# Kernel tuning notes

Hardware: AMD Instinct MI355X
Metric: run time of the kernel (lower is better)

The kernel has to match this reference:

```python
import jax, jax.numpy as jnp
import numpy as np

N = 50000      # nodes
E = 800000     # edges (before self-loops)
IN = 256       # input features
H = 8          # heads
C = 32         # hidden channels per head
OUT = 40       # classes
NEG_SLOPE = 0.2


def setup_inputs() -> dict:
    key = jax.random.key(0)
    ks = jax.random.split(key, 12)
    sd = lambda k, sh: (jax.random.normal(k, sh, jnp.float32) * 0.05)
    return {
        "x": jax.random.normal(ks[0], (N, IN), jnp.float32),
        "edge_index": jax.random.randint(ks[1], (2, E), 0, N),
        "W1": sd(ks[2], (IN, H * C)),
        "a_src1": sd(ks[3], (H, C)),
        "a_dst1": sd(ks[4], (H, C)),
        "b1": jnp.zeros((C,), jnp.float32),
        "W2": sd(ks[5], (C, H * C)),
        "a_src2": sd(ks[6], (H, C)),
        "a_dst2": sd(ks[7], (H, C)),
        "b2": jnp.zeros((C,), jnp.float32),
        "Wo": sd(ks[8], (C, OUT)),
        "bo": jnp.zeros((OUT,), jnp.float32),
    }


def gat_layer(x, src, dst, n, W, a_src, a_dst, b):
    # x: [N, F]; src/dst: [E'] (self-loops included). concat=False -> mean over heads.
    h = (x @ W).reshape(n, H, C)                       # [N, H, C]
    alpha_src = jnp.sum(h * a_src, axis=-1)            # [N, H]
    alpha_dst = jnp.sum(h * a_dst, axis=-1)            # [N, H]
    e = alpha_src[src] + alpha_dst[dst]                # [E', H]
    e = jnp.where(e > 0, e, NEG_SLOPE * e)             # leaky_relu
    # segment softmax over incoming edges of each dst node
    m = jax.ops.segment_max(e, dst, num_segments=n)    # [N, H]
    ex = jnp.exp(e - m[dst])                           # [E', H]
    s = jax.ops.segment_sum(ex, dst, num_segments=n)   # [N, H]
    alpha = ex / s[dst]                                # [E', H]
    msg = alpha[:, :, None] * h[src]                   # [E', H, C]
    out = jax.ops.segment_sum(msg, dst, num_segments=n)  # [N, H, C]
    return out.mean(axis=1) + b                        # [N, C]


def reference(x, edge_index, W1, a_src1, a_dst1, b1, W2, a_src2, a_dst2, b2, Wo, bo):
    n = x.shape[0]
    loops = jnp.arange(n, dtype=edge_index.dtype)
    src = jnp.concatenate([edge_index[0], loops])      # add self-loops (PyG default)
    dst = jnp.concatenate([edge_index[1], loops])
    h = gat_layer(x, src, dst, n, W1, a_src1, a_dst1, b1)
    h = jax.nn.elu(h)                                  # dropout skipped (eval)
    h = gat_layer(h, src, dst, n, W2, a_src2, a_dst2, b2)
    h = jax.nn.elu(h)
    logits = h @ Wo + bo
    return jax.nn.log_softmax(logits, axis=1)
```

## Files before the change

### kernel.cpp

```cpp
#include <hip/hip_runtime.h>
#include <math.h>

#define N_NODES 50000
#define N_PAD   50016
#define N_EDGES 800000
#define E_TOT   (N_EDGES + N_NODES)
#define F_IN    256
#define NHEAD   8
#define CH      32
#define HC      256
#define OUT_C   40
#define NEG_SLOPE 0.2f
#define SCAN_BLOCKS ((N_NODES + 255) / 256)
#define G_XCVT  ((N_NODES * F_IN / 8 + 255) / 256)
#define G_WCVT  ((HC * F_IN + 255) / 256)
#define G_WCVT2 ((HC * CH + 255) / 256)

typedef unsigned short u16;
typedef unsigned int   u32;
typedef unsigned char  u8;
typedef __attribute__((ext_vector_type(8))) short bf16x8;
typedef __attribute__((ext_vector_type(4))) float f32x4;
typedef __attribute__((ext_vector_type(2))) float f32x2;

__device__ __forceinline__ u16 f2bf(float f) {
    union { u32 u; float f; } x; x.f = f;
    u32 u = x.u;
    return (u16)((u + 0x7fffu + ((u >> 16) & 1u)) >> 16);
}
__device__ __forceinline__ float bflo(u32 v) {
    union { u32 u; float f; } x; x.u = v << 16; return x.f;
}
__device__ __forceinline__ u8 f2fp8(float f) {
    return (u8)(__builtin_amdgcn_cvt_pk_fp8_f32(f, f, 0, false) & 0xff);
}


__global__ __launch_bounds__(256) void cvt_kernel(const float* __restrict__ x,
        u16* __restrict__ xb, const float* __restrict__ W1, u16* __restrict__ Wt,
        const float* __restrict__ W2, u16* __restrict__ W2t) {
    int b = blockIdx.x;
    if (b < G_XCVT) {
        int t = b * 256 + threadIdx.x;
        if (t >= N_NODES * F_IN / 8) return;
        const float4* xp = (const float4*)x + (size_t)t * 2;
        float4 v0 = xp[0], v1 = xp[1];
        uint4 o;
        o.x = (u32)f2bf(v0.x) | ((u32)f2bf(v0.y) << 16);
        o.y = (u32)f2bf(v0.z) | ((u32)f2bf(v0.w) << 16);
        o.z = (u32)f2bf(v1.x) | ((u32)f2bf(v1.y) << 16);
        o.w = (u32)f2bf(v1.z) | ((u32)f2bf(v1.w) << 16);
        ((uint4*)xb)[t] = o;
    } else if (b < G_XCVT + G_WCVT) {
        int t = (b - G_XCVT) * 256 + threadIdx.x;
        int n = t & 255, k = t >> 8;
        Wt[(size_t)n * F_IN + k] = f2bf(W1[(size_t)k * HC + n]);
    } else {
        int t = (b - G_XCVT - G_WCVT) * 256 + threadIdx.x;
        if (t >= HC * CH) return;
        int n = t & 255, k = t >> 8;
        W2t[(size_t)n * CH + k] = f2bf(W2[(size_t)k * HC + n]);
    }
}

__global__ __launch_bounds__(256) void gemm1_mfma(const u16* __restrict__ xb,
        const u16* __restrict__ Wt, u8* __restrict__ ht8) {
    const int row0 = blockIdx.x * 32;
    const int t    = threadIdx.x;
    const int wave = t >> 6;
    const int lane = t & 63;
    const int l16  = lane & 15;
    const int quad = lane >> 4;
    const int nb   = wave * 64;

    f32x4 acc[2][4];
    #pragma unroll
    for (int m = 0; m < 2; ++m)
        #pragma unroll
        for (int n = 0; n < 4; ++n) acc[m][n] = (f32x4){0.f, 0.f, 0.f, 0.f};

    const u16* a0p = xb + (size_t)(row0 + l16) * F_IN;
    const u16* a1p = a0p + 16 * F_IN;
    const u16* bp  = Wt + (size_t)(nb + l16) * F_IN;

    #pragma unroll 1
    for (int k0 = 0; k0 < F_IN; k0 += 32) {
        const int ko = k0 + quad * 8;
        bf16x8 a0 = *(const bf16x8*)(a0p + ko);
        bf16x8 a1 = *(const bf16x8*)(a1p + ko);
        bf16x8 b0 = *(const bf16x8*)(bp + 0 * 16 * F_IN + ko);
        bf16x8 b1 = *(const bf16x8*)(bp + 1 * 16 * F_IN + ko);
        bf16x8 b2 = *(const bf16x8*)(bp + 2 * 16 * F_IN + ko);
        bf16x8 b3 = *(const bf16x8*)(bp + 3 * 16 * F_IN + ko);
        acc[0][0] = __builtin_amdgcn_mfma_f32_16x16x32_bf16(a0, b0, acc[0][0], 0, 0, 0);
        acc[0][1] = __builtin_amdgcn_mfma_f32_16x16x32_bf16(a0, b1, acc[0][1], 0, 0, 0);
        acc[0][2] = __builtin_amdgcn_mfma_f32_16x16x32_bf16(a0, b2, acc[0][2], 0, 0, 0);
        acc[0][3] = __builtin_amdgcn_mfma_f32_16x16x32_bf16(a0, b3, acc[0][3], 0, 0, 0);
        acc[1][0] = __builtin_amdgcn_mfma_f32_16x16x32_bf16(a1, b0, acc[1][0], 0, 0, 0);
        acc[1][1] = __builtin_amdgcn_mfma_f32_16x16x32_bf16(a1, b1, acc[1][1], 0, 0, 0);
        acc[1][2] = __builtin_amdgcn_mfma_f32_16x16x32_bf16(a1, b2, acc[1][2], 0, 0, 0);
        acc[1][3] = __builtin_amdgcn_mfma_f32_16x16x32_bf16(a1, b3, acc[1][3], 0, 0, 0);
    }

    #pragma unroll
    for (int m = 0; m < 2; ++m) {
        #pragma unroll
        for (int r = 0; r < 4; ++r) {
            int row = row0 + m * 16 + quad * 4 + r;
            if (row < N_NODES) {
                u8* hr = ht8 + (size_t)row * HC;
                #pragma unroll
                for (int n = 0; n < 4; ++n) {
                    int col = nb + n * 16 + l16;
                    hr[col] = f2fp8(acc[m][n][r]);
                }
            }
        }
    }
}

__global__ __launch_bounds__(256) void gemm2_mfma(const u16* __restrict__ hmb,
        const u16* __restrict__ W2t, u8* __restrict__ ht8) {
    const int row0 = blockIdx.x * 32;
    const int t    = threadIdx.x;
    const int wave = t >> 6;
    const int lane = t & 63;
    const int l16  = lane & 15;
    const int quad = lane >> 4;
    const int nb   = wave * 64;
    const int ko   = quad * 8;

    const u16* a0p = hmb + (size_t)(row0 + l16) * CH;
    const u16* a1p = a0p + 16 * CH;
    const u16* bp  = W2t + (size_t)(nb + l16) * CH;

    bf16x8 a0 = *(const bf16x8*)(a0p + ko);
    bf16x8 a1 = *(const bf16x8*)(a1p + ko);
    bf16x8 b0 = *(const bf16x8*)(bp + 0 * 16 * CH + ko);
    bf16x8 b1 = *(const bf16x8*)(bp + 1 * 16 * CH + ko);
    bf16x8 b2 = *(const bf16x8*)(bp + 2 * 16 * CH + ko);
    bf16x8 b3 = *(const bf16x8*)(bp + 3 * 16 * CH + ko);

    f32x4 z = (f32x4){0.f, 0.f, 0.f, 0.f};
    f32x4 acc[2][4];
    acc[0][0] = __builtin_amdgcn_mfma_f32_16x16x32_bf16(a0, b0, z, 0, 0, 0);
    acc[0][1] = __builtin_amdgcn_mfma_f32_16x16x32_bf16(a0, b1, z, 0, 0, 0);
    acc[0][2] = __builtin_amdgcn_mfma_f32_16x16x32_bf16(a0, b2, z, 0, 0, 0);
    acc[0][3] = __builtin_amdgcn_mfma_f32_16x16x32_bf16(a0, b3, z, 0, 0, 0);
    acc[1][0] = __builtin_amdgcn_mfma_f32_16x16x32_bf16(a1, b0, z, 0, 0, 0);
    acc[1][1] = __builtin_amdgcn_mfma_f32_16x16x32_bf16(a1, b1, z, 0, 0, 0);
    acc[1][2] = __builtin_amdgcn_mfma_f32_16x16x32_bf16(a1, b2, z, 0, 0, 0);
    acc[1][3] = __builtin_amdgcn_mfma_f32_16x16x32_bf16(a1, b3, z, 0, 0, 0);

    #pragma unroll
    for (int m = 0; m < 2; ++m) {
        #pragma unroll
        for (int r = 0; r < 4; ++r) {
            int row = row0 + m * 16 + quad * 4 + r;
            if (row < N_NODES) {
                u8* hr = ht8 + (size_t)row * HC;
                #pragma unroll
                for (int n = 0; n < 4; ++n) {
                    int col = nb + n * 16 + l16;
                    hr[col] = f2fp8(acc[m][n][r]);
                }
            }
        }
    }
}

__global__ __launch_bounds__(256) void alpha_t_kernel(const u8* __restrict__ ht8,
        const float* __restrict__ a_src, const float* __restrict__ a_dst,
        float* __restrict__ asrc, float* __restrict__ adst) {
    __shared__ float sas[HC], sad[HC];
    for (int i = threadIdx.x; i < HC; i += 256) {
        sas[i] = a_src[i];
        sad[i] = a_dst[i];
    }
    __syncthreads();
    int node = blockIdx.x * 256 + threadIdx.x;
    if (node >= N_NODES) return;
    const uint2* hp = (const uint2*)(ht8 + (size_t)node * HC);
    float s1[NHEAD], s2[NHEAD];
    #pragma unroll
    for (int h = 0; h < NHEAD; ++h) {
        float t1 = 0.f, t2 = 0.f;
        #pragma unroll
        for (int i = 0; i < 4; ++i) {
            uint2 v = hp[h * 4 + i];
            f32x2 p01 = __builtin_amdgcn_cvt_pk_f32_fp8(v.x, false);
            f32x2 p23 = __builtin_amdgcn_cvt_pk_f32_fp8(v.x, true);
            f32x2 p45 = __builtin_amdgcn_cvt_pk_f32_fp8(v.y, false);
            f32x2 p67 = __builtin_amdgcn_cvt_pk_f32_fp8(v.y, true);
            const float* s1p = &sas[h * CH + i * 8];
            const float* s2p = &sad[h * CH + i * 8];
            t1 += p01.x * s1p[0] + p01.y * s1p[1] + p23.x * s1p[2] + p23.y * s1p[3]
                + p45.x * s1p[4] + p45.y * s1p[5] + p67.x * s1p[6] + p67.y * s1p[7];
            t2 += p01.x * s2p[0] + p01.y * s2p[1] + p23.x * s2p[2] + p23.y * s2p[3]
                + p45.x * s2p[4] + p45.y * s2p[5] + p67.x * s2p[6] + p67.y * s2p[7];
        }
        s1[h] = t1; s2[h] = t2;
    }
    float4* o1 = (float4*)(asrc + (size_t)node * NHEAD);
    float4* o2 = (float4*)(adst + (size_t)node * NHEAD);
    o1[0] = make_float4(s1[0], s1[1], s1[2], s1[3]);
    o1[1] = make_float4(s1[4], s1[5], s1[6], s1[7]);
    o2[0] = make_float4(s2[0], s2[1], s2[2], s2[3]);
    o2[1] = make_float4(s2[4], s2[5], s2[6], s2[7]);
}

__global__ __launch_bounds__(256) void deg_kernel(const int* __restrict__ ei,
        int* __restrict__ deg) {
    int j = blockIdx.x * 256 + threadIdx.x;
    if (j >= E_TOT) return;
    int dst = (j < N_EDGES) ? ei[N_EDGES + j] : (j - N_EDGES);
    atomicAdd(&deg[dst], 1);
}

__device__ __forceinline__ int wave_incl_scan(int v, int lane) {
    #pragma unroll
    for (int d = 1; d < 64; d <<= 1) {
        int u = __shfl_up(v, d, 64);
        if (lane >= d) v += u;
    }
    return v;
}

__global__ __launch_bounds__(256) void scan1_kernel(const int* __restrict__ deg,
        int* __restrict__ rowptr, int* __restrict__ partials) {
    const int t    = blockIdx.x * 256 + threadIdx.x;
    const int lane = threadIdx.x & 63;
    const int wid  = threadIdx.x >> 6;
    int v = (t < N_NODES) ? deg[t] : 0;
    int inc = wave_incl_scan(v, lane);
    __shared__ int wtot[4];
    if (lane == 63) wtot[wid] = inc;
    __syncthreads();
    int woff = 0;
    #pragma unroll
    for (int i = 0; i < 4; ++i) woff += (i < wid) ? wtot[i] : 0;
    if (t < N_NODES) rowptr[t] = inc - v + woff;
    if (threadIdx.x == 255) partials[blockIdx.x] = woff + inc;
}

__global__ __launch_bounds__(256) void scan2_kernel(int* __restrict__ partials) {
    const int t    = threadIdx.x;
    const int lane = t & 63;
    const int wid  = t >> 6;
    int v = (t < SCAN_BLOCKS) ? partials[t] : 0;
    int inc = wave_incl_scan(v, lane);
    __shared__ int wtot[4];
    if (lane == 63) wtot[wid] = inc;
    __syncthreads();
    int woff = 0;
    #pragma unroll
    for (int i = 0; i < 4; ++i) woff += (i < wid) ? wtot[i] : 0;
    __syncthreads();
    if (t < SCAN_BLOCKS) partials[t] = inc - v + woff;
}

__global__ __launch_bounds__(256) void scan3_kernel(int* __restrict__ rowptr,
        int* __restrict__ cursor, const int* __restrict__ partials) {
    const int t = blockIdx.x * 256 + threadIdx.x;
    if (t < N_NODES) {
        int v = rowptr[t] + partials[blockIdx.x];
        rowptr[t] = v;
        cursor[t] = v;
    } else if (t == N_NODES) {
        rowptr[N_NODES] = E_TOT;
    }
}

__global__ __launch_bounds__(256) void scatter_kernel(const int* __restrict__ ei,
        int* __restrict__ cursor, int* __restrict__ csr_src) {
    int j = blockIdx.x * 256 + threadIdx.x;
    if (j >= E_TOT) return;
    int src, dst;
    if (j < N_EDGES) { src = ei[j]; dst = ei[N_EDGES + j]; }
    else             { src = j - N_EDGES; dst = src; }
    int pos = atomicAdd(&cursor[dst], 1);
    csr_src[pos] = src;
}

__global__ __launch_bounds__(256) void attn_kernel(const int* __restrict__ rowptr,
        const int* __restrict__ csr_src, const float* __restrict__ asrc,
        const float* __restrict__ adst, const u8* __restrict__ ht8,
        const float* __restrict__ b, u16* __restrict__ out) {
    const int wid = (blockIdx.x * 256 + threadIdx.x) >> 6;
    if (wid >= N_NODES) return;
    const int dst  = wid;
    const int lane = threadIdx.x & 63;
    const int q    = lane >> 4;
    const int l16  = lane & 15;
    const int h    = l16 >> 1;
    const float ad_own = adst[dst * NHEAD + h];

    float acc[16];
    #pragma unroll
    for (int i = 0; i < 16; ++i) acc[i] = 0.f;
    float wsum = 0.f;

    auto consume = [&](float as_, const uint4& hv) {
        float x = as_ + ad_own;
        x = x > 0.f ? x : NEG_SLOPE * x;
        float w = __expf(x);
        wsum += w;
        f32x2 d;
        d = __builtin_amdgcn_cvt_pk_f32_fp8(hv.x, false); acc[ 0] += w * d.x; acc[ 1] += w * d.y;
        d = __builtin_amdgcn_cvt_pk_f32_fp8(hv.x, true ); acc[ 2] += w * d.x; acc[ 3] += w * d.y;
        d = __builtin_amdgcn_cvt_pk_f32_fp8(hv.y, false); acc[ 4] += w * d.x; acc[ 5] += w * d.y;
        d = __builtin_amdgcn_cvt_pk_f32_fp8(hv.y, true ); acc[ 6] += w * d.x; acc[ 7] += w * d.y;
        d = __builtin_amdgcn_cvt_pk_f32_fp8(hv.z, false); acc[ 8] += w * d.x; acc[ 9] += w * d.y;
        d = __builtin_amdgcn_cvt_pk_f32_fp8(hv.z, true ); acc[10] += w * d.x; acc[11] += w * d.y;
        d = __builtin_amdgcn_cvt_pk_f32_fp8(hv.w, false); acc[12] += w * d.x; acc[13] += w * d.y;
        d = __builtin_amdgcn_cvt_pk_f32_fp8(hv.w, true ); acc[14] += w * d.x; acc[15] += w * d.y;
    };

    const int p0 = rowptr[dst], p1 = rowptr[dst + 1];
    const int boff = l16 * 16;

    float asA = 0.f, asB = 0.f;
    uint4 hvA = make_uint4(0u, 0u, 0u, 0u), hvB = make_uint4(0u, 0u, 0u, 0u);
    int eA = p0 + q;
    int eB = eA + 4;
    if (eA < p1) {
        int s = csr_src[eA];
        asA = asrc[s * NHEAD + h];
        hvA = *(const uint4*)(ht8 + (size_t)s * HC + boff);
    }
    if (eB < p1) {
        int s = csr_src[eB];
        asB = asrc[s * NHEAD + h];
        hvB = *(const uint4*)(ht8 + (size_t)s * HC + boff);
    }

    while (eA < p1) {
        consume(asA, hvA);
        if (eA + 8 < p1) {
            int s = csr_src[eA + 8];
            asA = asrc[s * NHEAD + h];
            hvA = *(const uint4*)(ht8 + (size_t)s * HC + boff);
        }
        if (eB < p1) consume(asB, hvB);
        if (eB + 8 < p1) {
            int s = csr_src[eB + 8];
            asB = asrc[s * NHEAD + h];
            hvB = *(const uint4*)(ht8 + (size_t)s * HC + boff);
        }
        eA += 8; eB += 8;
    }

    #pragma unroll
    for (int i = 0; i < 16; ++i) {
        acc[i] += __shfl_xor(acc[i], 16, 64);
        acc[i] += __shfl_xor(acc[i], 32, 64);
    }
    wsum += __shfl_xor(wsum, 16, 64);
    wsum += __shfl_xor(wsum, 32, 64);

    float winv = 1.0f / wsum;
    #pragma unroll
    for (int i = 0; i < 16; ++i) acc[i] *= winv;

    #pragma unroll
    for (int i = 0; i < 16; ++i) {
        acc[i] += __shfl_xor(acc[i], 2, 64);
        acc[i] += __shfl_xor(acc[i], 4, 64);
        acc[i] += __shfl_xor(acc[i], 8, 64);
    }

    if (lane < 2) {
        const int c0 = lane * 16;
        const float4* bp4 = (const float4*)(b + c0);
        float4 b0 = bp4[0], b1 = bp4[1], b2 = bp4[2], b3 = bp4[3];
        float bb[16] = {b0.x, b0.y, b0.z, b0.w, b1.x, b1.y, b1.z, b1.w,
                        b2.x, b2.y, b2.z, b2.w, b3.x, b3.y, b3.z, b3.w};
        u32 d[8];
        #pragma unroll
        for (int i = 0; i < 8; ++i) {
            float v0 = acc[2 * i]     * 0.125f + bb[2 * i];
            float v1 = acc[2 * i + 1] * 0.125f + bb[2 * i + 1];
            v0 = v0 > 0.f ? v0 : (__expf(v0) - 1.f);
            v1 = v1 > 0.f ? v1 : (__expf(v1) - 1.f);
            d[i] = (u32)f2bf(v0) | ((u32)f2bf(v1) << 16);
        }
        uint4* op = (uint4*)(out + (size_t)dst * CH + c0);
        op[0] = make_uint4(d[0], d[1], d[2], d[3]);
        op[1] = make_uint4(d[4], d[5], d[6], d[7]);
    }
}

__global__ __launch_bounds__(256) void out_kernel(const u16* __restrict__ hf,
        const float* __restrict__ Wo, const float* __restrict__ bo,
        float* __restrict__ out) {
    const int wave = threadIdx.x >> 6;
    const int lane = threadIdx.x & 63;
    const int n    = blockIdx.x * 4 + wave;
    __shared__ float hs[4][CH];
    if (n < N_NODES && lane < CH) hs[wave][lane] = bflo((u32)hf[n * CH + lane]);
    __syncthreads();
    if (n >= N_NODES) return;
    float logit = -INFINITY;
    if (lane < OUT_C) {
        float a = bo[lane];
        #pragma unroll
        for (int k = 0; k < CH; ++k) a += hs[wave][k] * Wo[k * OUT_C + lane];
        logit = a;
    }
    float m = logit;
    #pragma unroll
    for (int off = 32; off; off >>= 1) m = fmaxf(m, __shfl_xor(m, off, 64));
    float ex = (lane < OUT_C) ? __expf(logit - m) : 0.f;
    float ssum = ex;
    #pragma unroll
    for (int off = 32; off; off >>= 1) ssum += __shfl_xor(ssum, off, 64);
    if (lane < OUT_C) out[(size_t)n * OUT_C + lane] = logit - m - __logf(ssum);
}

extern "C" void kernel_launch(void* const* d_in, const int* in_sizes, int n_in,
                              void* d_out, int out_size, void* d_ws, size_t ws_size,
                              hipStream_t stream) {
    const float* x      = (const float*)d_in[0];
    const int*   ei     = (const int*)  d_in[1];
    const float* W1     = (const float*)d_in[2];
    const float* a_src1 = (const float*)d_in[3];
    const float* a_dst1 = (const float*)d_in[4];
    const float* b1     = (const float*)d_in[5];
    const float* W2     = (const float*)d_in[6];
    const float* a_src2 = (const float*)d_in[7];
    const float* a_dst2 = (const float*)d_in[8];
    const float* b2     = (const float*)d_in[9];
    const float* Wo     = (const float*)d_in[10];
    const float* bo     = (const float*)d_in[11];
    float* out = (float*)d_out;

    char* ws = (char*)d_ws;
    size_t off = 0;
    auto carve = [&](size_t bytes) { char* p = ws + off; off += (bytes + 255) & ~(size_t)255; return p; };
    u8*    ht8     = (u8*)   carve((size_t)N_NODES * HC);
    u16*   xb      = (u16*)  carve((size_t)N_PAD * F_IN * 2);
    u16*   Wt      = (u16*)  carve((size_t)HC * F_IN * 2);
    u16*   W2t     = (u16*)  carve((size_t)HC * CH * 2);
    float* asrc    = (float*)carve((size_t)N_NODES * NHEAD * 4);
    float* adst    = (float*)carve((size_t)N_NODES * NHEAD * 4);
    u16*   hmid    = (u16*)  carve((size_t)N_PAD * CH * 2);
    u16*   hout    = (u16*)  carve((size_t)N_NODES * CH * 2);
    int*   deg     = (int*)  carve((size_t)N_NODES * 4);
    int*   rowptr  = (int*)  carve((size_t)(N_NODES + 1) * 4);
    int*   cursor  = (int*)  carve((size_t)N_NODES * 4);
    int*   csr_src = (int*)  carve((size_t)E_TOT * 4);
    int*   partials= (int*)  carve((size_t)SCAN_BLOCKS * 4);

    const int g_cvt   = G_XCVT + G_WCVT + G_WCVT2;
    const int g_gemm  = (N_NODES + 31) / 32;
    const int g_node  = (N_NODES + 255) / 256;
    const int g_edge  = (E_TOT + 255) / 256;
    const int g_attn  = (N_NODES * 64 + 255) / 256;
    const int g_out   = (N_NODES + 3) / 4;

    cvt_kernel<<<g_cvt, 256, 0, stream>>>(x, xb, W1, Wt, W2, W2t);
    (void)hipMemsetAsync(deg, 0, (size_t)N_NODES * 4, stream);
    deg_kernel<<<g_edge, 256, 0, stream>>>(ei, deg);
    scan1_kernel<<<SCAN_BLOCKS, 256, 0, stream>>>(deg, rowptr, partials);
    scan2_kernel<<<1, 256, 0, stream>>>(partials);
    scan3_kernel<<<SCAN_BLOCKS, 256, 0, stream>>>(rowptr, cursor, partials);
    scatter_kernel<<<g_edge, 256, 0, stream>>>(ei, cursor, csr_src);

    gemm1_mfma<<<g_gemm, 256, 0, stream>>>(xb, Wt, ht8);
    alpha_t_kernel<<<g_node, 256, 0, stream>>>(ht8, a_src1, a_dst1, asrc, adst);
    attn_kernel<<<g_attn, 256, 0, stream>>>(rowptr, csr_src, asrc, adst, ht8, b1, hmid);

    gemm2_mfma<<<g_gemm, 256, 0, stream>>>(hmid, W2t, ht8);
    alpha_t_kernel<<<g_node, 256, 0, stream>>>(ht8, a_src2, a_dst2, asrc, adst);
    attn_kernel<<<g_attn, 256, 0, stream>>>(rowptr, csr_src, asrc, adst, ht8, b2, hout);

    out_kernel<<<g_out, 256, 0, stream>>>(hout, Wo, bo, out);
}
```

Measured before the change: 394.4 us.

## Fuse degree count into convert kernel, use 16-bit CSR indices, pack attention FMAs

The edge-degree atomic count now runs as extra blocks inside the input conversion kernel, which removes one launch and lets the two independent jobs overlap. CSR source indices are stored as 16-bit values, halving the index traffic that the attention gathers read; this depends on the node count fitting below 65536. The attention loop becomes a fixed-trip loop with two prefetched edges per step. Missing edges are padded with a very large negative score so their weight comes out as zero, and the feature accumulation uses packed two-wide FMAs to cut VALU instructions.

Measured after the change: 383.0 us. 2.9% less time.

```diff
diff --git a/kernel.cpp b/kernel.cpp
--- a/kernel.cpp
+++ b/kernel.cpp
@@ -12,6 +12,7 @@
 #define OUT_C   40
 #define NEG_SLOPE 0.2f
 #define SCAN_BLOCKS ((N_NODES + 255) / 256)
+#define G_DEG   ((E_TOT + 255) / 256)
 #define G_XCVT  ((N_NODES * F_IN / 8 + 255) / 256)
 #define G_WCVT  ((HC * F_IN + 255) / 256)
 #define G_WCVT2 ((HC * CH + 255) / 256)
@@ -38,10 +39,16 @@
 
 __global__ __launch_bounds__(256) void cvt_kernel(const float* __restrict__ x,
         u16* __restrict__ xb, const float* __restrict__ W1, u16* __restrict__ Wt,
-        const float* __restrict__ W2, u16* __restrict__ W2t) {
+        const float* __restrict__ W2, u16* __restrict__ W2t,
+        const int* __restrict__ ei, int* __restrict__ deg) {
     int b = blockIdx.x;
-    if (b < G_XCVT) {
-        int t = b * 256 + threadIdx.x;
+    if (b < G_DEG) {
+        int j = b * 256 + threadIdx.x;
+        if (j >= E_TOT) return;
+        int dstn = (j < N_EDGES) ? ei[N_EDGES + j] : (j - N_EDGES);
+        atomicAdd(&deg[dstn], 1);
+    } else if (b < G_DEG + G_XCVT) {
+        int t = (b - G_DEG) * 256 + threadIdx.x;
         if (t >= N_NODES * F_IN / 8) return;
         const float4* xp = (const float4*)x + (size_t)t * 2;
         float4 v0 = xp[0], v1 = xp[1];
@@ -51,12 +58,12 @@
         o.z = (u32)f2bf(v1.x) | ((u32)f2bf(v1.y) << 16);
         o.w = (u32)f2bf(v1.z) | ((u32)f2bf(v1.w) << 16);
         ((uint4*)xb)[t] = o;
-    } else if (b < G_XCVT + G_WCVT) {
-        int t = (b - G_XCVT) * 256 + threadIdx.x;
+    } else if (b < G_DEG + G_XCVT + G_WCVT) {
+        int t = (b - G_DEG - G_XCVT) * 256 + threadIdx.x;
         int n = t & 255, k = t >> 8;
         Wt[(size_t)n * F_IN + k] = f2bf(W1[(size_t)k * HC + n]);
     } else {
-        int t = (b - G_XCVT - G_WCVT) * 256 + threadIdx.x;
+        int t = (b - G_DEG - G_XCVT - G_WCVT) * 256 + threadIdx.x;
         if (t >= HC * CH) return;
         int n = t & 255, k = t >> 8;
         W2t[(size_t)n * CH + k] = f2bf(W2[(size_t)k * HC + n]);
@@ -209,14 +216,6 @@
     o2[1] = make_float4(s2[4], s2[5], s2[6], s2[7]);
 }
 
-__global__ __launch_bounds__(256) void deg_kernel(const int* __restrict__ ei,
-        int* __restrict__ deg) {
-    int j = blockIdx.x * 256 + threadIdx.x;
-    if (j >= E_TOT) return;
-    int dst = (j < N_EDGES) ? ei[N_EDGES + j] : (j - N_EDGES);
-    atomicAdd(&deg[dst], 1);
-}
-
 __device__ __forceinline__ int wave_incl_scan(int v, int lane) {
     #pragma unroll
     for (int d = 1; d < 64; d <<= 1) {
@@ -272,18 +271,18 @@
 }
 
 __global__ __launch_bounds__(256) void scatter_kernel(const int* __restrict__ ei,
-        int* __restrict__ cursor, int* __restrict__ csr_src) {
+        int* __restrict__ cursor, u16* __restrict__ csr_src) {
     int j = blockIdx.x * 256 + threadIdx.x;
     if (j >= E_TOT) return;
     int src, dst;
     if (j < N_EDGES) { src = ei[j]; dst = ei[N_EDGES + j]; }
     else             { src = j - N_EDGES; dst = src; }
     int pos = atomicAdd(&cursor[dst], 1);
-    csr_src[pos] = src;
+    csr_src[pos] = (u16)src;
 }
 
 __global__ __launch_bounds__(256) void attn_kernel(const int* __restrict__ rowptr,
-        const int* __restrict__ csr_src, const float* __restrict__ asrc,
+        const u16* __restrict__ csr_src, const float* __restrict__ asrc,
         const float* __restrict__ adst, const u8* __restrict__ ht8,
         const float* __restrict__ b, u16* __restrict__ out) {
     const int wid = (blockIdx.x * 256 + threadIdx.x) >> 6;
@@ -294,79 +293,100 @@
     const int l16  = lane & 15;
     const int h    = l16 >> 1;
     const float ad_own = adst[dst * NHEAD + h];
-
-    float acc[16];
-    #pragma unroll
-    for (int i = 0; i < 16; ++i) acc[i] = 0.f;
+    const u8* hbase = ht8 + l16 * 16;
+
+    f32x2 acc2[8];
+    #pragma unroll
+    for (int i = 0; i < 8; ++i) acc2[i] = (f32x2){0.f, 0.f};
     float wsum = 0.f;
 
-    auto consume = [&](float as_, const uint4& hv) {
-        float x = as_ + ad_own;
-        x = x > 0.f ? x : NEG_SLOPE * x;
-        float w = __expf(x);
-        wsum += w;
-        f32x2 d;
-        d = __builtin_amdgcn_cvt_pk_f32_fp8(hv.x, false); acc[ 0] += w * d.x; acc[ 1] += w * d.y;
-        d = __builtin_amdgcn_cvt_pk_f32_fp8(hv.x, true ); acc[ 2] += w * d.x; acc[ 3] += w * d.y;
-        d = __builtin_amdgcn_cvt_pk_f32_fp8(hv.y, false); acc[ 4] += w * d.x; acc[ 5] += w * d.y;
-        d = __builtin_amdgcn_cvt_pk_f32_fp8(hv.y, true ); acc[ 6] += w * d.x; acc[ 7] += w * d.y;
-        d = __builtin_amdgcn_cvt_pk_f32_fp8(hv.z, false); acc[ 8] += w * d.x; acc[ 9] += w * d.y;
-        d = __builtin_amdgcn_cvt_pk_f32_fp8(hv.z, true ); acc[10] += w * d.x; acc[11] += w * d.y;
-        d = __builtin_amdgcn_cvt_pk_f32_fp8(hv.w, false); acc[12] += w * d.x; acc[13] += w * d.y;
-        d = __builtin_amdgcn_cvt_pk_f32_fp8(hv.w, true ); acc[14] += w * d.x; acc[15] += w * d.y;
-    };
-
     const int p0 = rowptr[dst], p1 = rowptr[dst + 1];
-    const int boff = l16 * 16;
-
-    float asA = 0.f, asB = 0.f;
+    const int nt = (p1 - p0 + 7) >> 3;
+
+    float asA = -1e30f, asB = -1e30f;
     uint4 hvA = make_uint4(0u, 0u, 0u, 0u), hvB = make_uint4(0u, 0u, 0u, 0u);
-    int eA = p0 + q;
-    int eB = eA + 4;
-    if (eA < p1) {
-        int s = csr_src[eA];
+    int e = p0 + q;
+    if (e < p1) {
+        int s = (int)csr_src[e];
         asA = asrc[s * NHEAD + h];
-        hvA = *(const uint4*)(ht8 + (size_t)s * HC + boff);
-    }
-    if (eB < p1) {
-        int s = csr_src[eB];
+        hvA = *(const uint4*)(hbase + ((size_t)s << 8));
+    }
+    if (e + 4 < p1) {
+        int s = (int)csr_src[e + 4];
         asB = asrc[s * NHEAD + h];
-        hvB = *(const uint4*)(ht8 + (size_t)s * HC + boff);
-    }
-
-    while (eA < p1) {
-        consume(asA, hvA);
-        if (eA + 8 < p1) {
-            int s = csr_src[eA + 8];
+        hvB = *(const uint4*)(hbase + ((size_t)s << 8));
+    }
+
+    for (int it = 0; it < nt; ++it) {
+        float aA = asA; uint4 hA = hvA;
+        float aB = asB; uint4 hB = hvB;
+        asA = -1e30f; asB = -1e30f;
+        if (e + 8 < p1) {
+            int s = (int)csr_src[e + 8];
             asA = asrc[s * NHEAD + h];
-            hvA = *(const uint4*)(ht8 + (size_t)s * HC + boff);
-        }
-        if (eB < p1) consume(asB, hvB);
-        if (eB + 8 < p1) {
-            int s = csr_src[eB + 8];
+            hvA = *(const uint4*)(hbase + ((size_t)s << 8));
+        }
+        if (e + 12 < p1) {
+            int s = (int)csr_src[e + 12];
             asB = asrc[s * NHEAD + h];
-            hvB = *(const uint4*)(ht8 + (size_t)s * HC + boff);
-        }
-        eA += 8; eB += 8;
-    }
-
-    #pragma unroll
-    for (int i = 0; i < 16; ++i) {
-        acc[i] += __shfl_xor(acc[i], 16, 64);
-        acc[i] += __shfl_xor(acc[i], 32, 64);
+            hvB = *(const uint4*)(hbase + ((size_t)s << 8));
+        }
+        {
+            float x = aA + ad_own;
+            x = x > 0.f ? x : NEG_SLOPE * x;
+            float w = __expf(x);
+            wsum += w;
+            f32x2 w2; w2.x = w; w2.y = w;
+            acc2[0] = __builtin_elementwise_fma(w2, __builtin_amdgcn_cvt_pk_f32_fp8(hA.x, false), acc2[0]);
+            acc2[1] = __builtin_elementwise_fma(w2, __builtin_amdgcn_cvt_pk_f32_fp8(hA.x, true ), acc2[1]);
+            acc2[2] = __builtin_elementwise_fma(w2, __builtin_amdgcn_cvt_pk_f32_fp8(hA.y, false), acc2[2]);
+            acc2[3] = __builtin_elementwise_fma(w2, __builtin_amdgcn_cvt_pk_f32_fp8(hA.y, true ), acc2[3]);
+            acc2[4] = __builtin_elementwise_fma(w2, __builtin_amdgcn_cvt_pk_f32_fp8(hA.z, false), acc2[4]);
+            acc2[5] = __builtin_elementwise_fma(w2, __builtin_amdgcn_cvt_pk_f32_fp8(hA.z, true ), acc2[5]);
+            acc2[6] = __builtin_elementwise_fma(w2, __builtin_amdgcn_cvt_pk_f32_fp8(hA.w, false), acc2[6]);
+            acc2[7] = __builtin_elementwise_fma(w2, __builtin_amdgcn_cvt_pk_f32_fp8(hA.w, true ), acc2[7]);
+        }
+        {
+            float x = aB + ad_own;
+            x = x > 0.f ? x : NEG_SLOPE * x;
+            float w = __expf(x);
+            wsum += w;
+            f32x2 w2; w2.x = w; w2.y = w;
+            acc2[0] = __builtin_elementwise_fma(w2, __builtin_amdgcn_cvt_pk_f32_fp8(hB.x, false), acc2[0]);
+            acc2[1] = __builtin_elementwise_fma(w2, __builtin_amdgcn_cvt_pk_f32_fp8(hB.x, true ), acc2[1]);
+            acc2[2] = __builtin_elementwise_fma(w2, __builtin_amdgcn_cvt_pk_f32_fp8(hB.y, false), acc2[2]);
+            acc2[3] = __builtin_elementwise_fma(w2, __builtin_amdgcn_cvt_pk_f32_fp8(hB.y, true ), acc2[3]);
+            acc2[4] = __builtin_elementwise_fma(w2, __builtin_amdgcn_cvt_pk_f32_fp8(hB.z, false), acc2[4]);
+            acc2[5] = __builtin_elementwise_fma(w2, __builtin_amdgcn_cvt_pk_f32_fp8(hB.z, true ), acc2[5]);
+            acc2[6] = __builtin_elementwise_fma(w2, __builtin_amdgcn_cvt_pk_f32_fp8(hB.w, false), acc2[6]);
+            acc2[7] = __builtin_elementwise_fma(w2, __builtin_amdgcn_cvt_pk_f32_fp8(hB.w, true ), acc2[7]);
+        }
+        e += 8;
+    }
+
+    #pragma unroll
+    for (int i = 0; i < 8; ++i) {
+        acc2[i].x += __shfl_xor(acc2[i].x, 16, 64);
+        acc2[i].y += __shfl_xor(acc2[i].y, 16, 64);
+        acc2[i].x += __shfl_xor(acc2[i].x, 32, 64);
+        acc2[i].y += __shfl_xor(acc2[i].y, 32, 64);
     }
     wsum += __shfl_xor(wsum, 16, 64);
     wsum += __shfl_xor(wsum, 32, 64);
 
     float winv = 1.0f / wsum;
-    #pragma unroll
-    for (int i = 0; i < 16; ++i) acc[i] *= winv;
-
-    #pragma unroll
-    for (int i = 0; i < 16; ++i) {
-        acc[i] += __shfl_xor(acc[i], 2, 64);
-        acc[i] += __shfl_xor(acc[i], 4, 64);
-        acc[i] += __shfl_xor(acc[i], 8, 64);
+    f32x2 winv2; winv2.x = winv; winv2.y = winv;
+    #pragma unroll
+    for (int i = 0; i < 8; ++i) acc2[i] *= winv2;
+
+    #pragma unroll
+    for (int i = 0; i < 8; ++i) {
+        acc2[i].x += __shfl_xor(acc2[i].x, 2, 64);
+        acc2[i].y += __shfl_xor(acc2[i].y, 2, 64);
+        acc2[i].x += __shfl_xor(acc2[i].x, 4, 64);
+        acc2[i].y += __shfl_xor(acc2[i].y, 4, 64);
+        acc2[i].x += __shfl_xor(acc2[i].x, 8, 64);
+        acc2[i].y += __shfl_xor(acc2[i].y, 8, 64);
     }
 
     if (lane < 2) {
@@ -378,8 +398,8 @@
         u32 d[8];
         #pragma unroll
         for (int i = 0; i < 8; ++i) {
-            float v0 = acc[2 * i]     * 0.125f + bb[2 * i];
-            float v1 = acc[2 * i + 1] * 0.125f + bb[2 * i + 1];
+            float v0 = acc2[i].x * 0.125f + bb[2 * i];
+            float v1 = acc2[i].y * 0.125f + bb[2 * i + 1];
             v0 = v0 > 0.f ? v0 : (__expf(v0) - 1.f);
             v1 = v1 > 0.f ? v1 : (__expf(v1) - 1.f);
             d[i] = (u32)f2bf(v0) | ((u32)f2bf(v1) << 16);
@@ -448,19 +468,18 @@
     int*   deg     = (int*)  carve((size_t)N_NODES * 4);
     int*   rowptr  = (int*)  carve((size_t)(N_NODES + 1) * 4);
     int*   cursor  = (int*)  carve((size_t)N_NODES * 4);
-    int*   csr_src = (int*)  carve((size_t)E_TOT * 4);
+    u16*   csr_src = (u16*)  carve((size_t)E_TOT * 2);
     int*   partials= (int*)  carve((size_t)SCAN_BLOCKS * 4);
 
-    const int g_cvt   = G_XCVT + G_WCVT + G_WCVT2;
+    const int g_cvt   = G_DEG + G_XCVT + G_WCVT + G_WCVT2;
     const int g_gemm  = (N_NODES + 31) / 32;
     const int g_node  = (N_NODES + 255) / 256;
     const int g_edge  = (E_TOT + 255) / 256;
     const int g_attn  = (N_NODES * 64 + 255) / 256;
     const int g_out   = (N_NODES + 3) / 4;
 
-    cvt_kernel<<<g_cvt, 256, 0, stream>>>(x, xb, W1, Wt, W2, W2t);
     (void)hipMemsetAsync(deg, 0, (size_t)N_NODES * 4, stream);
-    deg_kernel<<<g_edge, 256, 0, stream>>>(ei, deg);
+    cvt_kernel<<<g_cvt, 256, 0, stream>>>(x, xb, W1, Wt, W2, W2t, ei, deg);
     scan1_kernel<<<SCAN_BLOCKS, 256, 0, stream>>>(deg, rowptr, partials);
     scan2_kernel<<<1, 256, 0, stream>>>(partials);
     scan3_kernel<<<SCAN_BLOCKS, 256, 0, stream>>>(rowptr, cursor, partials);
```
